# Kernel tuning notes

Hardware: AMD Instinct MI355X
Metric: run time of the kernel (lower is better)

Reference implementation:

```python
import jax, jax.numpy as jnp
import numpy as np

# Static rendering config (from init_kwargs)
H, W, D = 128, 128, 64          # image height, width, depth samples
PIXEL = 1.0                      # pixel size
EXTENT_Z = 128.0
DZ = EXTENT_Z / D                # z spacing = 2.0
HIDDEN = 64                      # field MLP hidden dim
MD, MH, MW = 128, 128, 128       # mask volume shape


def _axis(n, s):
    # arange(n) - n/2 + 0.5, scaled: centered grid axis (center_grid_origin=True)
    return (jnp.arange(n, dtype=jnp.float32) - n / 2 + 0.5) * s


def make_base_grid():
    # cartesian_prod(px, py, pz, [1]) reshaped to [H, W, D, 4] == meshgrid 'ij'
    px, py, pz = _axis(H, PIXEL), _axis(W, PIXEL), _axis(D, DZ)
    gx, gy, gz = jnp.meshgrid(px, py, pz, indexing='ij')
    return jnp.stack([gx, gy, gz, jnp.ones_like(gx)], axis=-1)  # [H,W,D,4]


def trilinear_zeros(vol, xyz):
    """torch F.grid_sample 3D, bilinear, padding_mode='zeros', align_corners=True.
    vol: [Dm,Hm,Wm]; xyz: [N,3] normalized coords in [-1,1], x indexes W, y->H, z->D."""
    Dm, Hm, Wm = vol.shape
    x = (xyz[:, 0] + 1.0) * 0.5 * (Wm - 1)
    y = (xyz[:, 1] + 1.0) * 0.5 * (Hm - 1)
    z = (xyz[:, 2] + 1.0) * 0.5 * (Dm - 1)
    x0, y0, z0 = jnp.floor(x), jnp.floor(y), jnp.floor(z)
    fx, fy, fz = x - x0, y - y0, z - z0
    out = jnp.zeros_like(x)
    for dz_ in (0, 1):
        for dy_ in (0, 1):
            for dx_ in (0, 1):
                xi, yi, zi = x0 + dx_, y0 + dy_, z0 + dz_
                w = ((fx if dx_ else 1.0 - fx)
                     * (fy if dy_ else 1.0 - fy)
                     * (fz if dz_ else 1.0 - fz))
                valid = ((xi >= 0) & (xi <= Wm - 1) & (yi >= 0) & (yi <= Hm - 1)
                         & (zi >= 0) & (zi <= Dm - 1))
                v = vol[jnp.clip(zi, 0, Dm - 1).astype(jnp.int32),
                        jnp.clip(yi, 0, Hm - 1).astype(jnp.int32),
                        jnp.clip(xi, 0, Wm - 1).astype(jnp.int32)]
                out = out + w * jnp.where(valid, v, 0.0)
    return out


def setup_inputs() -> dict:
    key = jax.random.key(0)
    k1, k2, k3, k4 = jax.random.split(key, 4)
    # rigid rotation (last row [0,0,0,1]) so homogeneous w stays 1
    th, ph = 0.3, 0.5
    c, s = np.cos(th), np.sin(th)
    c2, s2 = np.cos(ph), np.sin(ph)
    Rz = np.array([[c, -s, 0, 0], [s, c, 0, 0], [0, 0, 1, 0], [0, 0, 0, 1]], np.float32)
    Rx = np.array([[1, 0, 0, 0], [0, c2, -s2, 0], [0, s2, c2, 0], [0, 0, 0, 1]], np.float32)
    T = jnp.asarray(Rz @ Rx)[None]  # [1,4,4]
    mask_vol = (jax.random.uniform(k1, (MD, MH, MW)) > 0.4).astype(jnp.float32)
    W1 = jax.random.normal(k2, (3, HIDDEN), jnp.float32) * 0.5
    b1 = jax.random.normal(k3, (HIDDEN,), jnp.float32) * 0.1
    W2 = jax.random.normal(k4, (HIDDEN, 1), jnp.float32) * 0.2
    b2 = jnp.zeros((1,), jnp.float32)
    return {"transform_matrix": T, "mask_vol": mask_vol,
            "W1": W1, "b1": b1, "W2": W2, "b2": b2}


def reference(transform_matrix, mask_vol, W1, b1, W2, b2):
    base = make_base_grid().reshape(-1, 4)           # [N,4], N = H*W*D
    T = transform_matrix[0]                          # [4,4]
    q = base @ T.T                                   # transformed homogeneous points [N,4]
    # setup_masked_buffers: normalize to [-1,1] by max |coord| of the base grid
    max_abs = jnp.max(jnp.abs(base[:, :3]))
    norm_xyz = q[:, :3] / max_abs
    m_interp = trilinear_zeros(mask_vol, norm_xyz)   # trilinear mask sample [N]
    mask = (m_interp != 0).astype(jnp.float32)       # .to(torch.bool) cast
    # forward: homogeneous divide, field eval (masked points only; here mask-weighted)
    q3 = q[:, :3] / q[:, 3:4]                        # [N,3]
    h = jax.nn.relu(q3 @ W1 + b1)                    # [N,HIDDEN]
    pot = (h @ W2 + b2)[:, 0]                        # [N]
    # segment_sum_csr over contiguous depth bins == sum over z axis per pixel
    img = jnp.sum((pot * mask).reshape(H, W, D), axis=-1) * DZ  # [H,W]
    return img[None]                                 # [1,H,W] (batch 1)
```

## Files before the change

kernel.cpp:

```cpp
#include <hip/hip_runtime.h>


#define NH 128
#define NW 128
#define ND 64
#define HID 64

__global__ __launch_bounds__(256) void pack_kernel(
    const float* __restrict__ vol,
    unsigned long long* __restrict__ bits)
{
    const int t = blockIdx.x * 256 + threadIdx.x;
    const float v = vol[t];
    const unsigned long long b = __ballot(v != 0.0f);
    if ((threadIdx.x & 63) == 0)
        bits[t >> 6] = b;
}

__global__ __launch_bounds__(256) void dmp_kernel(
    const float* __restrict__ T,
    const unsigned int* __restrict__ bw,
    const float* __restrict__ W1,
    const float* __restrict__ b1,
    const float* __restrict__ W2,
    const float* __restrict__ b2,
    float* __restrict__ out)
{
    const int t   = blockIdx.x * 256 + threadIdx.x;
    const int d   = t & 63;
    const int pix = t >> 6;
    const int h   = pix >> 7;
    const int w   = pix & 127;

    const float bx = (float)h - 63.5f;
    const float by = (float)w - 63.5f;
    const float bz = ((float)d - 31.5f) * 2.0f;

    const float q0 = T[0]  * bx + T[1]  * by + T[2]  * bz + T[3];
    const float q1 = T[4]  * bx + T[5]  * by + T[6]  * bz + T[7];
    const float q2 = T[8]  * bx + T[9]  * by + T[10] * bz + T[11];
    const float qw = T[12] * bx + T[13] * by + T[14] * bz + T[15];

    const float inv_max = 1.0f / 63.5f;
    const float nx = q0 * inv_max;
    const float ny = q1 * inv_max;
    const float nz = q2 * inv_max;

    const float xf = (nx + 1.0f) * 0.5f * 127.0f;
    const float yf = (ny + 1.0f) * 0.5f * 127.0f;
    const float zf = (nz + 1.0f) * 0.5f * 127.0f;
    const float x0 = floorf(xf), y0 = floorf(yf), z0 = floorf(zf);
    const float fx = xf - x0, fy = yf - y0, fz = zf - z0;

    const bool lane_touch = (xf >= -1.0f) && (x0 <= 127.0f)
                         && (yf >= -1.0f) && (y0 <= 127.0f)
                         && (zf >= -1.0f) && (z0 <= 127.0f);

    float m = 0.0f;
    if (__any(lane_touch)) {
        #pragma unroll
        for (int dz_ = 0; dz_ < 2; ++dz_) {
            #pragma unroll
            for (int dy_ = 0; dy_ < 2; ++dy_) {
                #pragma unroll
                for (int dx_ = 0; dx_ < 2; ++dx_) {
                    const float xi = x0 + (float)dx_;
                    const float yi = y0 + (float)dy_;
                    const float zi = z0 + (float)dz_;
                    const float wgt = (dx_ ? fx : 1.0f - fx)
                                    * (dy_ ? fy : 1.0f - fy)
                                    * (dz_ ? fz : 1.0f - fz);
                    const bool valid = (xi >= 0.0f) && (xi <= 127.0f)
                                    && (yi >= 0.0f) && (yi <= 127.0f)
                                    && (zi >= 0.0f) && (zi <= 127.0f);
                    const int xc = min(max((int)xi, 0), 127);
                    const int yc = min(max((int)yi, 0), 127);
                    const int zc = min(max((int)zi, 0), 127);
                    const unsigned int word = bw[((zc << 7) + yc) * 4 + (xc >> 5)];
                    const bool bit = (word >> (xc & 31)) & 1u;
                    m += (valid && bit) ? wgt : 0.0f;
                }
            }
        }
    }
    const float mask = (m != 0.0f) ? 1.0f : 0.0f;

    float val = 0.0f;
    if (__any(mask != 0.0f)) {
        const float invw = 1.0f / qw;
        const float p0 = q0 * invw, p1 = q1 * invw, p2 = q2 * invw;
        float pot = b2[0];
        #pragma unroll 8
        for (int j = 0; j < HID; ++j) {
            float hj = p0 * W1[j] + p1 * W1[64 + j] + p2 * W1[128 + j] + b1[j];
            hj = fmaxf(hj, 0.0f);
            pot += hj * W2[j];
        }
        val = pot * mask;
    }

    #pragma unroll
    for (int off = 32; off > 0; off >>= 1)
        val += __shfl_down(val, off);

    if (d == 0)
        out[pix] = val * 2.0f;
}

extern "C" void kernel_launch(void* const* d_in, const int* in_sizes, int n_in,
                              void* d_out, int out_size, void* d_ws, size_t ws_size,
                              hipStream_t stream) {
    const float* T   = (const float*)d_in[0];
    const float* vol = (const float*)d_in[1];
    const float* W1  = (const float*)d_in[2];
    const float* b1  = (const float*)d_in[3];
    const float* W2  = (const float*)d_in[4];
    const float* b2  = (const float*)d_in[5];
    float* out = (float*)d_out;

    unsigned long long* bits = (unsigned long long*)d_ws;

    pack_kernel<<<8192, 256, 0, stream>>>(vol, bits);

    const int n_points = NH * NW * ND;
    dmp_kernel<<<n_points / 256, 256, 0, stream>>>(
        T, (const unsigned int*)bits, W1, b1, W2, b2, out);
}
```

Measured before the change: 86.88 us.

## Use dilated occupancy bitmap and closed-form ReLU depth sums per hidden unit

Adds a dilation kernel that ORs each voxel's 2x2x2 neighbourhood into a bitmap, so interior sample points resolve their mask with one bit lookup instead of eight. Only edge points fall back to the full trilinear check. The per-point MLP is replaced by a per-hidden-unit formulation: each lane owns one hidden unit, finds analytically the contiguous range of depth samples where that unit's pre-activation is positive, and sums the linear term in closed form with popcounts over the ballot mask. This assumes the homogeneous w equals 1 (it drops the divide) and adds an extra kernel launch.

```diff
diff --git a/kernel.cpp b/kernel.cpp
--- a/kernel.cpp
+++ b/kernel.cpp
@@ -17,38 +17,51 @@
         bits[t >> 6] = b;
 }
 
+__global__ __launch_bounds__(256) void dilate_kernel(
+    const unsigned long long* __restrict__ b,
+    unsigned long long* __restrict__ oc)
+{
+    const int r = blockIdx.x * 256 + threadIdx.x;
+    const int z = r >> 7, y = r & 127;
+    const int i = r << 1;
+    unsigned long long lo = b[i], hi = b[i + 1];
+    if (y < 127) { lo |= b[i + 2];   hi |= b[i + 3]; }
+    if (z < 127) {
+        lo |= b[i + 256]; hi |= b[i + 257];
+        if (y < 127) { lo |= b[i + 258]; hi |= b[i + 259]; }
+    }
+    oc[i]     = lo | (lo >> 1) | (hi << 63);
+    oc[i + 1] = hi | (hi >> 1);
+}
+
 __global__ __launch_bounds__(256) void dmp_kernel(
     const float* __restrict__ T,
     const unsigned int* __restrict__ bw,
+    const unsigned int* __restrict__ oc,
     const float* __restrict__ W1,
     const float* __restrict__ b1,
     const float* __restrict__ W2,
     const float* __restrict__ b2,
     float* __restrict__ out)
 {
-    const int t   = blockIdx.x * 256 + threadIdx.x;
-    const int d   = t & 63;
-    const int pix = t >> 6;
-    const int h   = pix >> 7;
-    const int w   = pix & 127;
+    const int t    = blockIdx.x * 256 + threadIdx.x;
+    const int lane = t & 63;
+    const int pix  = t >> 6;
+    const int h    = pix >> 7;
+    const int w    = pix & 127;
 
     const float bx = (float)h - 63.5f;
     const float by = (float)w - 63.5f;
-    const float bz = ((float)d - 31.5f) * 2.0f;
+    const float bz = ((float)lane - 31.5f) * 2.0f;
 
-    const float q0 = T[0]  * bx + T[1]  * by + T[2]  * bz + T[3];
-    const float q1 = T[4]  * bx + T[5]  * by + T[6]  * bz + T[7];
-    const float q2 = T[8]  * bx + T[9]  * by + T[10] * bz + T[11];
-    const float qw = T[12] * bx + T[13] * by + T[14] * bz + T[15];
+    const float q0 = T[0] * bx + T[1] * by + T[2]  * bz + T[3];
+    const float q1 = T[4] * bx + T[5] * by + T[6]  * bz + T[7];
+    const float q2 = T[8] * bx + T[9] * by + T[10] * bz + T[11];
 
     const float inv_max = 1.0f / 63.5f;
-    const float nx = q0 * inv_max;
-    const float ny = q1 * inv_max;
-    const float nz = q2 * inv_max;
-
-    const float xf = (nx + 1.0f) * 0.5f * 127.0f;
-    const float yf = (ny + 1.0f) * 0.5f * 127.0f;
-    const float zf = (nz + 1.0f) * 0.5f * 127.0f;
+    const float xf = (q0 * inv_max + 1.0f) * 0.5f * 127.0f;
+    const float yf = (q1 * inv_max + 1.0f) * 0.5f * 127.0f;
+    const float zf = (q2 * inv_max + 1.0f) * 0.5f * 127.0f;
     const float x0 = floorf(xf), y0 = floorf(yf), z0 = floorf(zf);
     const float fx = xf - x0, fy = yf - y0, fz = zf - z0;
 
@@ -56,8 +69,20 @@
                          && (yf >= -1.0f) && (y0 <= 127.0f)
                          && (zf >= -1.0f) && (z0 <= 127.0f);
 
+    const bool generic = (x0 >= 0.0f) && (x0 <= 126.0f) && (fx != 0.0f)
+                      && (y0 >= 0.0f) && (y0 <= 126.0f) && (fy != 0.0f)
+                      && (z0 >= 0.0f) && (z0 <= 126.0f) && (fz != 0.0f);
+
+    const int x0i = (int)x0, y0i = (int)y0, z0i = (int)z0;
+    const int xg = min(max(x0i, 0), 127);
+    const int yg = min(max(y0i, 0), 127);
+    const int zg = min(max(z0i, 0), 127);
+    const unsigned int ocw = oc[((zg << 7) + yg) * 4 + (xg >> 5)];
+    const bool ocbit = (ocw >> (xg & 31)) & 1u;
+
     float m = 0.0f;
-    if (__any(lane_touch)) {
+    const bool edge = lane_touch && !generic;
+    if (__any(edge)) {
         #pragma unroll
         for (int dz_ = 0; dz_ < 2; ++dz_) {
             #pragma unroll
@@ -78,33 +103,70 @@
                     const int zc = min(max((int)zi, 0), 127);
                     const unsigned int word = bw[((zc << 7) + yc) * 4 + (xc >> 5)];
                     const bool bit = (word >> (xc & 31)) & 1u;
-                    m += (valid && bit) ? wgt : 0.0f;
+                    m += (edge && valid && bit) ? wgt : 0.0f;
                 }
             }
         }
     }
-    const float mask = (m != 0.0f) ? 1.0f : 0.0f;
+    const bool masked = generic ? ocbit : (m != 0.0f);
+    const unsigned long long M = __ballot(masked);
 
-    float val = 0.0f;
-    if (__any(mask != 0.0f)) {
-        const float invw = 1.0f / qw;
-        const float p0 = q0 * invw, p1 = q1 * invw, p2 = q2 * invw;
-        float pot = b2[0];
-        #pragma unroll 8
-        for (int j = 0; j < HID; ++j) {
-            float hj = p0 * W1[j] + p1 * W1[64 + j] + p2 * W1[128 + j] + b1[j];
-            hj = fmaxf(hj, 0.0f);
-            pot += hj * W2[j];
-        }
-        val = pot * mask;
+    if (M == 0ull) {
+        if (lane == 0) out[pix] = 0.0f;
+        return;
     }
+
+    const int j = lane;
+    const float w0 = W1[j], w1 = W1[64 + j], w2 = W1[128 + j];
+    const float A  = w0 * T[0] + w1 * T[4] + w2 * T[8];
+    const float B  = w0 * T[1] + w1 * T[5] + w2 * T[9];
+    const float C  = w0 * T[2] + w1 * T[6] + w2 * T[10];
+    const float D0 = w0 * T[3] + w1 * T[7] + w2 * T[11] + b1[j];
+    const float u  = A * bx + B * by - 63.0f * C + D0;
+    const float g  = C + C;
+
+    unsigned long long rmask;
+    if (g > 0.0f) {
+        const float tt = __fdividef(-u, g);
+        int d0 = (int)floorf(tt) + 1;
+        d0 = min(max(d0, 0), 64);
+        if (d0 > 0 && fmaf(g, (float)(d0 - 1), u) > 0.0f)       d0 -= 1;
+        else if (d0 < 64 && fmaf(g, (float)d0, u) <= 0.0f)      d0 += 1;
+        rmask = (d0 >= 64) ? 0ull : (~0ull << d0);
+    } else if (g < 0.0f) {
+        const float tt = __fdividef(-u, g);
+        int d1 = (int)floorf(tt);
+        d1 = min(max(d1, -1), 63);
+        if (d1 < 63 && fmaf(g, (float)(d1 + 1), u) > 0.0f)      d1 += 1;
+        else if (d1 >= 0 && fmaf(g, (float)d1, u) <= 0.0f)      d1 -= 1;
+        rmask = (d1 < 0) ? 0ull : (~0ull >> (63 - d1));
+    } else {
+        rmask = (u > 0.0f) ? ~0ull : 0ull;
+    }
+
+    const unsigned long long R = rmask & M;
+    const unsigned int rlo = (unsigned int)R;
+    const unsigned int rhi = (unsigned int)(R >> 32);
+    const int N = __popc(rlo) + __popc(rhi);
+    int Dsum = __popc(rlo & 0xAAAAAAAAu)        + (__popc(rlo & 0xCCCCCCCCu) << 1)
+             + (__popc(rlo & 0xF0F0F0F0u) << 2) + (__popc(rlo & 0xFF00FF00u) << 3)
+             + (__popc(rlo & 0xFFFF0000u) << 4);
+    Dsum += __popc(rhi & 0xAAAAAAAAu)        + (__popc(rhi & 0xCCCCCCCCu) << 1)
+          + (__popc(rhi & 0xF0F0F0F0u) << 2) + (__popc(rhi & 0xFF00FF00u) << 3)
+          + (__popc(rhi & 0xFFFF0000u) << 4) + (__popc(rhi) << 5);
+
+    const float S = u * (float)N + g * (float)Dsum;
+    float val = W2[j] * S;
 
     #pragma unroll
     for (int off = 32; off > 0; off >>= 1)
         val += __shfl_down(val, off);
 
-    if (d == 0)
-        out[pix] = val * 2.0f;
+    if (lane == 0) {
+        const float nm = (float)(__popc((unsigned int)M)
+                               + __popc((unsigned int)(M >> 32)));
+        out[pix] = (val + b2[0] * nm) * 2.0f;
+    }
 }
 
 extern "C" void kernel_launch(void* const* d_in, const int* in_sizes, int n_in,
@@ -119,10 +181,13 @@
     float* out = (float*)d_out;
 
     unsigned long long* bits = (unsigned long long*)d_ws;
+    unsigned long long* oc   = (unsigned long long*)((char*)d_ws + 262144);
 
     pack_kernel<<<8192, 256, 0, stream>>>(vol, bits);
+    dilate_kernel<<<64, 256, 0, stream>>>(bits, oc);
 
     const int n_points = NH * NW * ND;
     dmp_kernel<<<n_points / 256, 256, 0, stream>>>(
-        T, (const unsigned int*)bits, W1, b1, W2, b2, out);
+        T, (const unsigned int*)bits, (const unsigned int*)oc,
+        W1, b1, W2, b2, out);
 }
```

Result: slower. 89.03 us (+2.5%).
